# Performance work log

Hardware: AMD Instinct MI355X
Metric: run time of the kernel (lower is better)

## Reference

```python
import jax, jax.numpy as jnp
import numpy as np

N, F_IN, F_OUT = 10000, 256, 64
ALPHA = 0.2  # LeakyReLU negative slope
NEG_BIG = -9e15  # matches -9000000000000000.0 in the torch code


def setup_inputs() -> dict:
    key = jax.random.key(0)
    k1, k2, k3, k4 = jax.random.split(key, 4)
    h = jax.random.normal(k1, (N, F_IN), dtype=jnp.float32)
    adj = jax.random.randint(k2, (N, N), 0, 2, dtype=jnp.int32)
    # xavier-uniform-like scales for params
    W = jax.random.normal(k3, (F_IN, F_OUT), dtype=jnp.float32) * 0.08
    a = jax.random.normal(k4, (2 * F_OUT, 1), dtype=jnp.float32) * 0.1
    return {"h": h, "adj": adj, "W": W, "a": a}


def reference(h, adj, W, a):
    # Wh: [N, F_OUT]
    Wh = h @ W
    # Additive attention: e_ij = LeakyReLU(a1 . Wh_i + a2 . Wh_j)
    # This is mathematically identical to matmul([Wh_i || Wh_j], a) without
    # materializing the [N, N, 2*F_OUT] tensor.
    f1 = Wh @ a[:F_OUT]        # [N, 1] -> contribution of source node i
    f2 = Wh @ a[F_OUT:]        # [N, 1] -> contribution of target node j
    e = f1 + f2.T              # [N, N]
    e = jnp.where(e > 0, e, ALPHA * e)          # LeakyReLU
    e = jnp.where(adj > 0, e, NEG_BIG)          # adjacency masking
    attention = jax.nn.softmax(e, axis=1)       # masked softmax over neighbors
    # dropout is a no-op in eval mode (training=False)
    h_prime = attention @ Wh                    # [N, F_OUT]
    return jax.nn.elu(h_prime)                  # concat=True -> ELU
```

## Files before the change

### kernel.cpp

```cpp
#include <hip/hip_runtime.h>
#include <hip/hip_bf16.h>

#define N_NODES  10000
#define NPAD     10240
#define FIN      256
#define D        64
#define NT256    40
#define ROWTILES 625
#define NSPLIT   4
#define ALPHA    0.2f

typedef __attribute__((ext_vector_type(8))) short bf16x8;
typedef __attribute__((ext_vector_type(4))) float f32x4;
typedef __attribute__((ext_vector_type(4))) int   i32x4;

__device__ __forceinline__ unsigned bf16bits(float x) {
  union { __hip_bfloat16 b; unsigned short s; } u;
  u.b = __float2bfloat16(x);
  return (unsigned)u.s;
}

__global__ __launch_bounds__(256) void k1_proj(
    const float* __restrict__ h, const float* __restrict__ W,
    const float* __restrict__ a,
    float* __restrict__ f1, float* __restrict__ f2,
    short* __restrict__ whT) {
  int wid  = (blockIdx.x << 2) + (threadIdx.x >> 6);
  int lane = threadIdx.x & 63;
  if (wid >= N_NODES) {
    if (wid < NPAD) whT[(size_t)lane * NPAD + wid] = 0;
    return;
  }
  const float* hrow = h + (size_t)wid * FIN;
  float s0 = 0.f, s1 = 0.f, s2 = 0.f, s3 = 0.f;
#pragma unroll 4
  for (int k = 0; k < FIN; k += 4) {
    float4 hv = *(const float4*)(hrow + k);
    s0 += hv.x * W[(k + 0) * D + lane];
    s1 += hv.y * W[(k + 1) * D + lane];
    s2 += hv.z * W[(k + 2) * D + lane];
    s3 += hv.w * W[(k + 3) * D + lane];
  }
  float acc = (s0 + s1) + (s2 + s3);
  whT[(size_t)lane * NPAD + wid] = (short)bf16bits(acc);
  float p1 = acc * a[lane];
  float p2 = acc * a[D + lane];
#pragma unroll
  for (int off = 32; off; off >>= 1) {
    p1 += __shfl_xor(p1, off);
    p2 += __shfl_xor(p2, off);
  }
  if (lane == 0) { f1[wid] = p1; f2[wid] = p2; }
}

__global__ __launch_bounds__(256) void k1b_max(
    const float* __restrict__ f2, float* __restrict__ f2maxF) {
  float m = -3.4e38f;
  for (int i = threadIdx.x; i < N_NODES; i += 256) m = fmaxf(m, f2[i]);
#pragma unroll
  for (int off = 32; off; off >>= 1) m = fmaxf(m, __shfl_xor(m, off));
  __shared__ float wm[4];
  if ((threadIdx.x & 63) == 0) wm[threadIdx.x >> 6] = m;
  __syncthreads();
  if (threadIdx.x == 0)
    *f2maxF = fmaxf(fmaxf(wm[0], wm[1]), fmaxf(wm[2], wm[3]));
}

__global__ __launch_bounds__(256) void k2_attn(
    const int* __restrict__ adj, const float* __restrict__ f1,
    const float* __restrict__ f2, const float* __restrict__ f2maxF,
    const short* __restrict__ whT,
    float* __restrict__ accP, float* __restrict__ sP) {
  __shared__ float ldsF[4096];
  char* ldsB = (char*)ldsF;
  int tid = threadIdx.x;
  int rowtile = blockIdx.x % ROWTILES;
  int split   = blockIdx.x / ROWTILES;

  int prow  = tid >> 4;
  int cbase = (tid & 15) * 4;
  int grow  = rowtile * 16 + prow;
  float f1r  = f1[grow];
  float mraw = f1r + *f2maxF;
  float Mhat = fmaxf(mraw, ALPHA * mraw);
  const int* adjrow = adj + (size_t)grow * N_NODES;

  int lane = tid & 63;
  int w    = tid >> 6;
  int r2   = lane & 15;
  int g    = lane >> 4;

  f32x4 acc[4];
#pragma unroll
  for (int cb = 0; cb < 4; ++cb) acc[cb] = (f32x4){0.f, 0.f, 0.f, 0.f};
  float sth = 0.f;

  int pboff[4];
#pragma unroll
  for (int sub = 0; sub < 4; ++sub)
    pboff[sub] = (prow * 512 + (cbase + sub * 64) * 2) ^ ((prow & 7) << 4);
  int cboff[2];
#pragma unroll
  for (int ks = 0; ks < 2; ++ks)
    cboff[ks] = (r2 * 512 + (w * 64 + ks * 32 + g * 8) * 2) ^ ((r2 & 7) << 4);
  const short* bbase = whT + (size_t)r2 * NPAD + w * 64 + g * 8;

  for (int tt = split; tt < NT256; tt += NSPLIT) {
    int j0 = tt << 8;
    i32x4 av[4]; f32x4 fv[4]; bool val[4];
#pragma unroll
    for (int sub = 0; sub < 4; ++sub) {
      int j = j0 + cbase + sub * 64;
      bool v = (j < N_NODES);
      int jc = v ? j : (N_NODES - 4);
      av[sub] = *(const i32x4*)(adjrow + jc);
      fv[sub] = *(const f32x4*)(f2 + jc);
      val[sub] = v;
    }
#pragma unroll
    for (int sub = 0; sub < 4; ++sub) {
      float p[4];
#pragma unroll
      for (int e = 0; e < 4; ++e) {
        float ev = f1r + fv[sub][e];
        ev = fmaxf(ev, ALPHA * ev);
        float pv = __expf(ev - Mhat);
        p[e] = (val[sub] && av[sub][e] != 0) ? pv : 0.f;
        sth += p[e];
      }
      uint2 pk;
      pk.x = bf16bits(p[0]) | (bf16bits(p[1]) << 16);
      pk.y = bf16bits(p[2]) | (bf16bits(p[3]) << 16);
      *(uint2*)(ldsB + pboff[sub]) = pk;
    }
    __syncthreads();
#pragma unroll
    for (int ks = 0; ks < 2; ++ks) {
      bf16x8 af = *(const bf16x8*)(ldsB + cboff[ks]);
      const short* bp = bbase + j0 + ks * 32;
#pragma unroll
      for (int cb = 0; cb < 4; ++cb) {
        bf16x8 bf = *(const bf16x8*)(bp + (size_t)cb * 16 * NPAD);
        acc[cb] = __builtin_amdgcn_mfma_f32_16x16x32_bf16(af, bf, acc[cb], 0, 0, 0);
      }
    }
    __syncthreads();
  }

  sth += __shfl_xor(sth, 1);
  sth += __shfl_xor(sth, 2);
  sth += __shfl_xor(sth, 4);
  sth += __shfl_xor(sth, 8);
  if ((tid & 15) == 0) sP[split * N_NODES + grow] = sth;

  float* accS = ldsF;
#pragma unroll
  for (int cb = 0; cb < 4; ++cb)
#pragma unroll
    for (int q = 0; q < 4; ++q)
      accS[(w * 16 + g * 4 + q) * 64 + cb * 16 + r2] = acc[cb][q];
  __syncthreads();
  int base = split * (N_NODES * D) + rowtile * 1024;
#pragma unroll
  for (int k = 0; k < 4; ++k) {
    int o = tid + k * 256;
    accP[base + o] = accS[o] + accS[1024 + o] + accS[2048 + o] + accS[3072 + o];
  }
}

__global__ __launch_bounds__(256) void k3_final(
    const float* __restrict__ accP, const float* __restrict__ sP,
    float* __restrict__ out) {
  int idx = blockIdx.x * 256 + threadIdx.x;
  if (idx >= N_NODES * D) return;
  int row = idx >> 6;
  float sv = (sP[row] + sP[N_NODES + row]) +
             (sP[2 * N_NODES + row] + sP[3 * N_NODES + row]);
  float v = ((accP[idx] + accP[640000 + idx]) +
             (accP[1280000 + idx] + accP[1920000 + idx])) / sv;
  out[idx] = v > 0.f ? v : (__expf(v) - 1.f);
}

extern "C" void kernel_launch(void* const* d_in, const int* in_sizes, int n_in,
                              void* d_out, int out_size, void* d_ws, size_t ws_size,
                              hipStream_t stream) {
  const float* h   = (const float*)d_in[0];
  const int*   adj = (const int*)d_in[1];
  const float* W   = (const float*)d_in[2];
  const float* a   = (const float*)d_in[3];
  float* out = (float*)d_out;

  float* wsf = (float*)d_ws;
  float* accP   = wsf;
  float* sP     = wsf + 2560000;
  float* f2maxF = wsf + 2600000;
  float* f1W    = wsf + 2600016;
  float* f2W    = wsf + 2610032;
  short* whT    = (short*)(wsf + 2620048);

  hipLaunchKernelGGL(k1_proj, dim3(NPAD / 4), dim3(256), 0, stream,
                     h, W, a, f1W, f2W, whT);
  hipLaunchKernelGGL(k1b_max, dim3(1), dim3(256), 0, stream, f2W, f2maxF);
  hipLaunchKernelGGL(k2_attn, dim3(ROWTILES * NSPLIT), dim3(256), 0, stream,
                     adj, f1W, f2W, f2maxF, whT, accP, sP);
  hipLaunchKernelGGL(k3_final, dim3((N_NODES * D + 255) / 256), dim3(256), 0, stream,
                     accP, sP, out);
}
```

Baseline: 638.4 us.

## Double-buffer attention tiles, prefetch next adjacency tile, halve column splits

Cuts the column-split count from four to two, which halves the partial accumulator traffic read by the final reduction kernel. The attention kernel now loads the next tile's adjacency and f2 values into registers while processing the current tile. It ping-pongs between two LDS buffers so the trailing barrier per iteration can be dropped. The trade-off is more registers and LDS per block, with only 1250 blocks left to fill the GPU.

```diff
diff --git a/kernel.cpp b/kernel.cpp
--- a/kernel.cpp
+++ b/kernel.cpp
@@ -7,7 +7,7 @@
 #define D        64
 #define NT256    40
 #define ROWTILES 625
-#define NSPLIT   4
+#define NSPLIT   2
 #define ALPHA    0.2f
 
 typedef __attribute__((ext_vector_type(8))) short bf16x8;
@@ -66,13 +66,12 @@
     *f2maxF = fmaxf(fmaxf(wm[0], wm[1]), fmaxf(wm[2], wm[3]));
 }
 
-__global__ __launch_bounds__(256) void k2_attn(
+__global__ __launch_bounds__(256, 4) void k2_attn(
     const int* __restrict__ adj, const float* __restrict__ f1,
     const float* __restrict__ f2, const float* __restrict__ f2maxF,
     const short* __restrict__ whT,
     float* __restrict__ accP, float* __restrict__ sP) {
-  __shared__ float ldsF[4096];
-  char* ldsB = (char*)ldsF;
+  __shared__ char ldsB[16384];
   int tid = threadIdx.x;
   int rowtile = blockIdx.x % ROWTILES;
   int split   = blockIdx.x / ROWTILES;
@@ -105,17 +104,31 @@
     cboff[ks] = (r2 * 512 + (w * 64 + ks * 32 + g * 8) * 2) ^ ((r2 & 7) << 4);
   const short* bbase = whT + (size_t)r2 * NPAD + w * 64 + g * 8;
 
+  i32x4 av[4]; f32x4 fv[4]; bool val[4];
+#pragma unroll
+  for (int sub = 0; sub < 4; ++sub) {
+    int j = (split << 8) + cbase + sub * 64;
+    bool v = (j < N_NODES);
+    int jc = v ? j : (N_NODES - 4);
+    av[sub] = *(const i32x4*)(adjrow + jc);
+    fv[sub] = *(const f32x4*)(f2 + jc);
+    val[sub] = v;
+  }
+
+  int cur = 0;
   for (int tt = split; tt < NT256; tt += NSPLIT) {
-    int j0 = tt << 8;
-    i32x4 av[4]; f32x4 fv[4]; bool val[4];
-#pragma unroll
-    for (int sub = 0; sub < 4; ++sub) {
-      int j = j0 + cbase + sub * 64;
-      bool v = (j < N_NODES);
-      int jc = v ? j : (N_NODES - 4);
-      av[sub] = *(const i32x4*)(adjrow + jc);
-      fv[sub] = *(const f32x4*)(f2 + jc);
-      val[sub] = v;
+    i32x4 av2[4]; f32x4 fv2[4]; bool val2[4];
+    int nt = tt + NSPLIT;
+    if (nt < NT256) {
+#pragma unroll
+      for (int sub = 0; sub < 4; ++sub) {
+        int j = (nt << 8) + cbase + sub * 64;
+        bool v = (j < N_NODES);
+        int jc = v ? j : (N_NODES - 4);
+        av2[sub] = *(const i32x4*)(adjrow + jc);
+        fv2[sub] = *(const f32x4*)(f2 + jc);
+        val2[sub] = v;
+      }
     }
 #pragma unroll
     for (int sub = 0; sub < 4; ++sub) {
@@ -131,12 +144,13 @@
       uint2 pk;
       pk.x = bf16bits(p[0]) | (bf16bits(p[1]) << 16);
       pk.y = bf16bits(p[2]) | (bf16bits(p[3]) << 16);
-      *(uint2*)(ldsB + pboff[sub]) = pk;
+      *(uint2*)(ldsB + (cur << 13) + pboff[sub]) = pk;
     }
     __syncthreads();
+    int j0 = tt << 8;
 #pragma unroll
     for (int ks = 0; ks < 2; ++ks) {
-      bf16x8 af = *(const bf16x8*)(ldsB + cboff[ks]);
+      bf16x8 af = *(const bf16x8*)(ldsB + (cur << 13) + cboff[ks]);
       const short* bp = bbase + j0 + ks * 32;
 #pragma unroll
       for (int cb = 0; cb < 4; ++cb) {
@@ -144,7 +158,11 @@
         acc[cb] = __builtin_amdgcn_mfma_f32_16x16x32_bf16(af, bf, acc[cb], 0, 0, 0);
       }
     }
-    __syncthreads();
+#pragma unroll
+    for (int sub = 0; sub < 4; ++sub) {
+      av[sub] = av2[sub]; fv[sub] = fv2[sub]; val[sub] = val2[sub];
+    }
+    cur ^= 1;
   }
 
   sth += __shfl_xor(sth, 1);
@@ -153,7 +171,8 @@
   sth += __shfl_xor(sth, 8);
   if ((tid & 15) == 0) sP[split * N_NODES + grow] = sth;
 
-  float* accS = ldsF;
+  __syncthreads();
+  float* accS = (float*)ldsB;
 #pragma unroll
   for (int cb = 0; cb < 4; ++cb)
 #pragma unroll
@@ -174,10 +193,8 @@
   int idx = blockIdx.x * 256 + threadIdx.x;
   if (idx >= N_NODES * D) return;
   int row = idx >> 6;
-  float sv = (sP[row] + sP[N_NODES + row]) +
-             (sP[2 * N_NODES + row] + sP[3 * N_NODES + row]);
-  float v = ((accP[idx] + accP[640000 + idx]) +
-             (accP[1280000 + idx] + accP[1920000 + idx])) / sv;
+  float sv = sP[row] + sP[N_NODES + row];
+  float v  = (accP[idx] + accP[640000 + idx]) / sv;
   out[idx] = v > 0.f ? v : (__expf(v) - 1.f);
 }
 
```

New measurement: 646.8 us. Within noise of the previous version (+1.3%).
